# Kernel optimization log

Hardware: AMD Instinct MI355X
Metric: run time of the kernel (lower is better)

The kernel has to match this reference:

```python
import jax, jax.numpy as jnp
import numpy as np

B, N, C, H = 8, 1568, 384, 6
D = C // H
SCALE = D ** -0.5
EPS = 1e-6


def setup_inputs() -> dict:
    key = jax.random.key(0)
    k1, k2, k3, k4 = jax.random.split(key, 4)
    x = jax.random.normal(k1, (B, N, C), dtype=jnp.float32)
    # binary token-keep policy (0/1), as produced by the pruning module
    vis_tube = jax.random.randint(k2, (B, N, 1), 0, 2).astype(jnp.float32)
    w_qkv = jax.random.normal(k3, (3 * C, C), dtype=jnp.float32) * (C ** -0.5)
    w_proj = jax.random.normal(k4, (C, C), dtype=jnp.float32) * (C ** -0.5)
    b_proj = jnp.zeros((C,), dtype=jnp.float32)
    return {"x": x, "vis_tube": vis_tube, "w_qkv": w_qkv, "w_proj": w_proj, "b_proj": b_proj}


def _attn_forward(x, vis_tube, w_qkv, w_proj, b_proj):
    qkv = (x @ w_qkv.T).reshape(B, N, 3, H, D)
    qkv = jnp.transpose(qkv, (2, 0, 3, 1, 4))  # [3,B,H,N,D]
    q, k, v = qkv[0], qkv[1], qkv[2]

    attn = jnp.einsum('bhnd,bhmd->bhnm', q, k) * SCALE  # [B,H,N,N]

    # softmax_with_policy: mask keys by policy, but always keep the diagonal
    policy = vis_tube.reshape(B, 1, 1, N)
    eye = jnp.eye(N, dtype=policy.dtype).reshape(1, 1, N, N)
    attn_policy = policy + (1.0 - policy) * eye  # [B,1,N,N]

    max_att = jnp.max(attn, axis=-1, keepdims=True)
    e = jnp.exp(attn - max_att) * attn_policy
    attn = (e + EPS / N) / (jnp.sum(e, axis=-1, keepdims=True) + EPS)

    out = jnp.einsum('bhnm,bhmd->bhnd', attn, v)  # [B,H,N,D]
    out = jnp.transpose(out, (0, 2, 1, 3)).reshape(B, N, C)
    return out @ w_proj.T + b_proj


def reference(x, vis_tube, w_qkv, w_proj, b_proj):
    return _attn_forward(x, vis_tube, w_qkv, w_proj, b_proj)
```

## Files before the change

kernel.cpp:

```cpp
#include <hip/hip_runtime.h>

#define B_ 8
#define N_ 1568
#define NPAD_ 1600
#define C_ 384
#define H_ 6
#define D_ 64
#define BH_ 48
#define SZ_ (B_*H_*N_*D_)
#define EPS_ 1e-6f
#define CSC_ 0.18033688011112042f

typedef short s16x8 __attribute__((ext_vector_type(8)));
typedef short s16x4 __attribute__((ext_vector_type(4)));
typedef float f32x4 __attribute__((ext_vector_type(4)));

static __device__ __forceinline__ ushort f2bf(float f){
  union { float f; unsigned u; } v; v.f = f;
  unsigned r = v.u + 0x7fffu + ((v.u >> 16) & 1u);
  return (ushort)(r >> 16);
}
static __device__ __forceinline__ unsigned cvtpk(float lo, float hi){
  unsigned r;
  asm("v_cvt_pk_bf16_f32 %0, %1, %2" : "=v"(r) : "v"(lo), "v"(hi));
  return r;
}
#define MFMA16(a,b,c) __builtin_amdgcn_mfma_f32_16x16x32_bf16((a),(b),(c),0,0,0)

#if __has_builtin(__builtin_amdgcn_exp2f)
#define EXP2F(x) __builtin_amdgcn_exp2f(x)
#else
#define EXP2F(x) exp2f(x)
#endif

#define POLPAD_ (B_*NPAD_)
__global__ __launch_bounds__(256) void pol_pad_k(const float* __restrict__ vis, float* __restrict__ pp){
  int i = blockIdx.x*256 + threadIdx.x;
  if (i < POLPAD_){
    int b = i / NPAD_, n = i - b*NPAD_;
    pp[i] = (n < N_) ? vis[b*N_ + n] : 0.f;
  }
}

#define XV8_ 602112
#define WQ8_ 55296
#define WP8_ 18432
__global__ __launch_bounds__(256) void cvt_all(const float* __restrict__ X, const float* __restrict__ Wq,
                                               const float* __restrict__ Wp, ushort* __restrict__ Xb,
                                               ushort* __restrict__ Wqb, ushort* __restrict__ Wpb){
  int i = blockIdx.x*256 + threadIdx.x;
  const float* src; ushort* dst; int off;
  if (i < XV8_)            { src = X;  dst = Xb;  off = i; }
  else if (i < XV8_+WQ8_)  { src = Wq; dst = Wqb; off = i - XV8_; }
  else                     { src = Wp; dst = Wpb; off = i - XV8_ - WQ8_; }
  float4 a = ((const float4*)src)[off*2];
  float4 b = ((const float4*)src)[off*2+1];
  s16x8 r;
  r[0]=(short)f2bf(a.x); r[1]=(short)f2bf(a.y); r[2]=(short)f2bf(a.z); r[3]=(short)f2bf(a.w);
  r[4]=(short)f2bf(b.x); r[5]=(short)f2bf(b.y); r[6]=(short)f2bf(b.z); r[7]=(short)f2bf(b.w);
  *(s16x8*)&dst[off*8] = r;
}

__global__ __launch_bounds__(256) void qkv_gemm(const ushort* __restrict__ Xb, const ushort* __restrict__ Wb,
                                                ushort* __restrict__ Qg, ushort* __restrict__ Kg,
                                                ushort* __restrict__ Vtg){
  __shared__ __align__(16) ushort Al[128*40];
  __shared__ __align__(16) ushort Bl[128*40];
  const int tid = threadIdx.x, lane = tid&63, w = tid>>6;
  const int g = lane>>4, lr = lane&15;
  const int wr = w>>1, wc = w&1;
  const int m0 = blockIdx.x*128, j0 = blockIdx.y*128;
  const int ar = tid>>1, ah = tid&1;
  f32x4 acc[4][4];
  #pragma unroll
  for (int i=0;i<4;i++)
    #pragma unroll
    for (int j=0;j<4;j++) acc[i][j]=(f32x4){0,0,0,0};

  for (int ks=0; ks<384; ks+=32){
    const ushort* as = Xb + (size_t)(m0+ar)*384 + ks + ah*16;
    s16x8 a0 = ((const s16x8*)as)[0];
    s16x8 a1 = ((const s16x8*)as)[1];
    const ushort* bs = Wb + (size_t)(j0+ar)*384 + ks + ah*16;
    s16x8 b0 = ((const s16x8*)bs)[0];
    s16x8 b1 = ((const s16x8*)bs)[1];
    *(s16x8*)&Al[ar*40 + ah*16]     = a0;
    *(s16x8*)&Al[ar*40 + ah*16 + 8] = a1;
    *(s16x8*)&Bl[ar*40 + ah*16]     = b0;
    *(s16x8*)&Bl[ar*40 + ah*16 + 8] = b1;
    __syncthreads();
    s16x8 af[4], bf[4];
    #pragma unroll
    for (int fm=0; fm<4; fm++) af[fm] = *(const s16x8*)&Al[(wr*64+fm*16+lr)*40 + g*8];
    #pragma unroll
    for (int fn=0; fn<4; fn++) bf[fn] = *(const s16x8*)&Bl[(wc*64+fn*16+lr)*40 + g*8];
    #pragma unroll
    for (int fm=0; fm<4; fm++)
      #pragma unroll
      for (int fn=0; fn<4; fn++)
        acc[fm][fn] = MFMA16(af[fm], bf[fn], acc[fm][fn]);
    __syncthreads();
  }
  #pragma unroll
  for (int fm=0; fm<4; fm++){
    #pragma unroll
    for (int jj=0; jj<4; jj++){
      int m = m0 + wr*64 + fm*16 + g*4 + jj;
      int bi = m / N_; int n = m - bi*N_;
      #pragma unroll
      for (int fn=0; fn<4; fn++){
        int j = j0 + wc*64 + fn*16 + lr;
        int t = j/384, jc = j - t*384;
        int h = jc>>6, d = jc&63;
        float v = acc[fm][fn][jj];
        if (t==0)      Qg[((size_t)(bi*H_+h)*N_ + n)*64 + d] = f2bf(v * CSC_);
        else if (t==1) Kg[((size_t)(bi*H_+h)*N_ + n)*64 + d] = f2bf(v);
        else           Vtg[((size_t)(bi*H_+h)*64 + d)*N_ + n] = f2bf(v);
      }
    }
  }
}

#define LOADK(D0,D1,TT) do{ \
  _Pragma("unroll") \
  for (int kg=0;kg<4;kg++){ \
    int kr = (TT)+kg*16+lr; kr = kr<N_?kr:N_-1; \
    const ushort* kp = Kbh + (size_t)kr*64; \
    D0[kg] = *(const s16x8*)(kp + g*8); \
    D1[kg] = *(const s16x8*)(kp + 32 + g*8); } }while(0)

#define LOADV(TT) do{ \
  _Pragma("unroll") \
  for (int fd=0;fd<4;fd++){ \
    const ushort* vp = Vbh + (size_t)(fd*16+lr)*N_ + (TT); \
    va0_[fd] = *(const s16x8*)(vp + g*8); \
    va1_[fd] = *(const s16x8*)(vp + 32 + g*8); } }while(0)

#define LOADP(TT) do{ \
  _Pragma("unroll") \
  for (int kg=0;kg<4;kg++) pmv[kg] = *(const float4*)&polp[(TT) + kg*16 + 4*g]; }while(0)

#define PROC(KC0,KC1,QF0,QF1,OO,MM,LL,QQ,DG,T0) do{ \
  f32x4 st[4]; \
  _Pragma("unroll") \
  for (int kg=0;kg<4;kg++){ f32x4 z=(f32x4){0,0,0,0}; z=MFMA16(KC0[kg],QF0,z); st[kg]=MFMA16(KC1[kg],QF1,z); } \
  float pmax; { \
    float x0=fmaxf(fmaxf(st[0][0],st[0][1]),fmaxf(st[0][2],st[0][3])); \
    float x1=fmaxf(fmaxf(st[1][0],st[1][1]),fmaxf(st[1][2],st[1][3])); \
    float x2=fmaxf(fmaxf(st[2][0],st[2][1]),fmaxf(st[2][2],st[2][3])); \
    float x3=fmaxf(fmaxf(st[3][0],st[3][1]),fmaxf(st[3][2],st[3][3])); \
    pmax=fmaxf(fmaxf(x0,x1),fmaxf(x2,x3)); \
    pmax=fmaxf(pmax,__shfl_xor(pmax,16)); pmax=fmaxf(pmax,__shfl_xor(pmax,32)); } \
  if (__any(pmax > (MM)+8.f)){ \
    float Mn=fmaxf((MM),pmax); float corr=EXP2F((MM)-Mn); (LL)*=corr; \
    _Pragma("unroll") for (int fd=0;fd<4;fd++){ OO[fd][0]*=corr;OO[fd][1]*=corr;OO[fd][2]*=corr;OO[fd][3]*=corr; } \
    (MM)=Mn; } \
  _Pragma("unroll") \
  for (int kg=0;kg<4;kg++){ \
    _Pragma("unroll") \
    for (int jj=0;jj<4;jj++){ \
      float e=EXP2F(st[kg][jj]-(MM)); float em=e*((&pmv[kg].x)[jj]); \
      int key=(T0)+kg*16+4*g+jj; \
      st[kg][jj]=((DG)&&key==(QQ))?e:em; } } \
  { float se=(st[0][0]+st[0][1])+(st[0][2]+st[0][3]); \
    se+=(st[1][0]+st[1][1])+(st[1][2]+st[1][3]); \
    se+=(st[2][0]+st[2][1])+(st[2][2]+st[2][3]); \
    se+=(st[3][0]+st[3][1])+(st[3][2]+st[3][3]); \
    se+=__shfl_xor(se,16); se+=__shfl_xor(se,32); (LL)+=se; } \
  unsigned pk[4][2]; \
  _Pragma("unroll") \
  for (int kg=0;kg<4;kg++){ pk[kg][0]=cvtpk(st[kg][0],st[kg][1]); pk[kg][1]=cvtpk(st[kg][2],st[kg][3]); } \
  union { unsigned u[4]; s16x8 v; } bfr[2]; \
  _Pragma("unroll") \
  for (int kh=0;kh<2;kh++){ \
    _Pragma("unroll") \
    for (int wd=0;wd<4;wd++){ \
      int srcl=(wd<2)?sl0:sl1; \
      unsigned q0_=(unsigned)__shfl((int)pk[2*kh][wd&1],srcl); \
      unsigned q1_=(unsigned)__shfl((int)pk[2*kh+1][wd&1],srcl); \
      bfr[kh].u[wd]=(g<2)?q0_:q1_; } } \
  _Pragma("unroll") \
  for (int fd=0;fd<4;fd++){ OO[fd]=MFMA16(va0_[fd],bfr[0].v,OO[fd]); OO[fd]=MFMA16(va1_[fd],bfr[1].v,OO[fd]); } \
}while(0)

__global__ __launch_bounds__(256,2) void attn_fwd(const ushort* __restrict__ Qg, const ushort* __restrict__ Kg,
                                                  const ushort* __restrict__ Vt, const float* __restrict__ pol,
                                                  ushort* __restrict__ AO){
  const int tid = threadIdx.x, lane = tid&63, w = tid>>6;
  const int g = lane>>4, lr = lane&15;
  const int bh = blockIdx.x; const int b = bh / H_, h = bh - b*H_;
  const int qbase = blockIdx.y*128 + w*32;
  const int qA = qbase + lr, qB = qbase + 16 + lr;
  const int qAc = qA < N_ ? qA : N_-1;
  const int qBc = qB < N_ ? qB : N_-1;
  const ushort* QrA = Qg + ((size_t)bh*N_ + qAc)*64;
  const ushort* QrB = Qg + ((size_t)bh*N_ + qBc)*64;
  const s16x8 qa0 = *(const s16x8*)(QrA + g*8);
  const s16x8 qa1 = *(const s16x8*)(QrA + 32 + g*8);
  const s16x8 qb0 = *(const s16x8*)(QrB + g*8);
  const s16x8 qb1 = *(const s16x8*)(QrB + 32 + g*8);
  const float* polp = pol + b*NPAD_;
  const ushort* Kbh = Kg + (size_t)bh*N_*64;
  const ushort* Vbh = Vt + (size_t)bh*64*N_;
  const int sl0 = ((lane>>4)&1)<<5 | lr;
  const int sl1 = sl0 + 16;
  const int dbase = qbase & ~63;

  f32x4 oA[4], oB[4];
  #pragma unroll
  for (int i=0;i<4;i++){ oA[i]=(f32x4){0,0,0,0}; oB[i]=(f32x4){0,0,0,0}; }
  float MA=-INFINITY, LA=0.f, MB=-INFINITY, LB=0.f;

  s16x8 ka0[4], ka1[4], kb0[4], kb1[4], va0_[4], va1_[4];
  float4 pmv[4];

  LOADK(ka0, ka1, 0);
  #pragma unroll 1
  for (int it=0; it<12; it++){
    const int t0 = it*128;
    LOADV(t0); LOADP(t0);
    LOADK(kb0, kb1, t0+64);
    PROC(ka0,ka1, qa0,qa1, oA,MA,LA,qA, (dbase==t0), t0);
    PROC(ka0,ka1, qb0,qb1, oB,MB,LB,qB, (dbase==t0), t0);
    const int t1 = t0+64;
    LOADV(t1); LOADP(t1);
    LOADK(ka0, ka1, t1+64);
    PROC(kb0,kb1, qa0,qa1, oA,MA,LA,qA, (dbase==t1), t1);
    PROC(kb0,kb1, qb0,qb1, oB,MB,LB,qB, (dbase==t1), t1);
  }
  {
    const int t0 = 1536;
    LOADV(t0); LOADP(t0);
    PROC(ka0,ka1, qa0,qa1, oA,MA,LA,qA, (dbase==t0), t0);
    PROC(ka0,ka1, qb0,qb1, oB,MB,LB,qB, (dbase==t0), t0);
  }

  if (qA < N_){
    float inv = 1.f / (LA + EPS_);
    ushort* aop = AO + ((size_t)b*N_ + qA)*C_ + h*64 + 4*g;
    #pragma unroll
    for (int fd=0; fd<4; fd++){
      s16x4 r;
      r[0]=(short)f2bf(oA[fd][0]*inv); r[1]=(short)f2bf(oA[fd][1]*inv);
      r[2]=(short)f2bf(oA[fd][2]*inv); r[3]=(short)f2bf(oA[fd][3]*inv);
      *(s16x4*)(aop + fd*16) = r;
    }
  }
  if (qB < N_){
    float inv = 1.f / (LB + EPS_);
    ushort* aop = AO + ((size_t)b*N_ + qB)*C_ + h*64 + 4*g;
    #pragma unroll
    for (int fd=0; fd<4; fd++){
      s16x4 r;
      r[0]=(short)f2bf(oB[fd][0]*inv); r[1]=(short)f2bf(oB[fd][1]*inv);
      r[2]=(short)f2bf(oB[fd][2]*inv); r[3]=(short)f2bf(oB[fd][3]*inv);
      *(s16x4*)(aop + fd*16) = r;
    }
  }
}

__global__ __launch_bounds__(256) void proj_gemm(const ushort* __restrict__ A, const ushort* __restrict__ Wb,
                                                 const float* __restrict__ bias, float* __restrict__ out){
  __shared__ __align__(16) ushort Al[128*40];
  __shared__ __align__(16) ushort Bl[128*40];
  const int tid = threadIdx.x, lane = tid&63, w = tid>>6;
  const int g = lane>>4, lr = lane&15;
  const int wr = w>>1, wc = w&1;
  const int m0 = blockIdx.x*128, j0 = blockIdx.y*128;
  const int ar = tid>>1, ah = tid&1;
  f32x4 acc[4][4];
  #pragma unroll
  for (int i=0;i<4;i++)
    #pragma unroll
    for (int j=0;j<4;j++) acc[i][j]=(f32x4){0,0,0,0};

  for (int ks=0; ks<384; ks+=32){
    const ushort* as = A + (size_t)(m0+ar)*384 + ks + ah*16;
    s16x8 a0 = ((const s16x8*)as)[0];
    s16x8 a1 = ((const s16x8*)as)[1];
    const ushort* bs = Wb + (size_t)(j0+ar)*384 + ks + ah*16;
    s16x8 b0 = ((const s16x8*)bs)[0];
    s16x8 b1 = ((const s16x8*)bs)[1];
    *(s16x8*)&Al[ar*40 + ah*16]     = a0;
    *(s16x8*)&Al[ar*40 + ah*16 + 8] = a1;
    *(s16x8*)&Bl[ar*40 + ah*16]     = b0;
    *(s16x8*)&Bl[ar*40 + ah*16 + 8] = b1;
    __syncthreads();
    s16x8 af[4], bf[4];
    #pragma unroll
    for (int fm=0; fm<4; fm++) af[fm] = *(const s16x8*)&Al[(wr*64+fm*16+lr)*40 + g*8];
    #pragma unroll
    for (int fn=0; fn<4; fn++) bf[fn] = *(const s16x8*)&Bl[(wc*64+fn*16+lr)*40 + g*8];
    #pragma unroll
    for (int fm=0; fm<4; fm++)
      #pragma unroll
      for (int fn=0; fn<4; fn++)
        acc[fm][fn] = MFMA16(af[fm], bf[fn], acc[fm][fn]);
    __syncthreads();
  }
  float bsv[4];
  #pragma unroll
  for (int fn=0; fn<4; fn++) bsv[fn] = bias[j0 + wc*64 + fn*16 + lr];
  #pragma unroll
  for (int fm=0; fm<4; fm++){
    #pragma unroll
    for (int jj=0; jj<4; jj++){
      int m = m0 + wr*64 + fm*16 + g*4 + jj;
      #pragma unroll
      for (int fn=0; fn<4; fn++){
        int j = j0 + wc*64 + fn*16 + lr;
        out[(size_t)m*384 + j] = acc[fm][fn][jj] + bsv[fn];
      }
    }
  }
}

extern "C" void kernel_launch(void* const* d_in, const int* in_sizes, int n_in,
                              void* d_out, int out_size, void* d_ws, size_t ws_size,
                              hipStream_t stream) {
  const float* x     = (const float*)d_in[0];
  const float* vis   = (const float*)d_in[1];
  const float* wqkv  = (const float*)d_in[2];
  const float* wproj = (const float*)d_in[3];
  const float* bproj = (const float*)d_in[4];
  float* out = (float*)d_out;

  ushort* Qg  = (ushort*)d_ws;
  ushort* Kg  = Qg + SZ_;
  ushort* Vtg = Kg + SZ_;
  ushort* AO  = Vtg + SZ_;
  ushort* Xb  = AO;
  ushort* Wqb = AO + SZ_;
  ushort* Wpb = Wqb + 3*C_*C_;
  float*  pol_pad = (float*)(Wpb + C_*C_);

  pol_pad_k<<<(POLPAD_+255)/256, 256, 0, stream>>>(vis, pol_pad);
  cvt_all<<<2640, 256, 0, stream>>>(x, wqkv, wproj, Xb, Wqb, Wpb);
  qkv_gemm<<<dim3(98,9), 256, 0, stream>>>(Xb, Wqb, Qg, Kg, Vtg);
  attn_fwd<<<dim3(48,13), 256, 0, stream>>>(Qg, Kg, Vtg, pol_pad, AO);
  proj_gemm<<<dim3(98,3), 256, 0, stream>>>(AO, Wpb, bproj, out);
}
```

Before: 253.6 us.

## Use single-wave attention blocks, add V transpose kernel, set MFMA priorities

The attention kernel goes from 256-thread blocks covering 128 queries to 64-thread blocks covering 32 queries, giving a 48x49 grid. Since 1568 = 49*32, the query bounds checks and clamps can be dropped. When the workspace is large enough, the QKV GEMM now writes V row-major and a separate small kernel transposes it through LDS, replacing the strided scattered Vt stores. The attention inner loop also gains s_setprio raises around the MFMA sections and sched_barrier fences after the loads. These changes add one extra kernel launch and a round-trip of V through memory.

```diff
diff --git a/kernel.cpp b/kernel.cpp
--- a/kernel.cpp
+++ b/kernel.cpp
@@ -63,7 +63,8 @@
 
 __global__ __launch_bounds__(256) void qkv_gemm(const ushort* __restrict__ Xb, const ushort* __restrict__ Wb,
                                                 ushort* __restrict__ Qg, ushort* __restrict__ Kg,
-                                                ushort* __restrict__ Vtg){
+                                                ushort* __restrict__ Vg, ushort* __restrict__ Vtg,
+                                                int vmode){
   __shared__ __align__(16) ushort Al[128*40];
   __shared__ __align__(16) ushort Bl[128*40];
   const int tid = threadIdx.x, lane = tid&63, w = tid>>6;
@@ -115,10 +116,27 @@
         float v = acc[fm][fn][jj];
         if (t==0)      Qg[((size_t)(bi*H_+h)*N_ + n)*64 + d] = f2bf(v * CSC_);
         else if (t==1) Kg[((size_t)(bi*H_+h)*N_ + n)*64 + d] = f2bf(v);
-        else           Vtg[((size_t)(bi*H_+h)*64 + d)*N_ + n] = f2bf(v);
+        else {
+          if (vmode) Vg[((size_t)(bi*H_+h)*N_ + n)*64 + d] = f2bf(v);
+          else       Vtg[((size_t)(bi*H_+h)*64 + d)*N_ + n] = f2bf(v);
+        }
       }
     }
   }
+}
+
+__global__ __launch_bounds__(256) void v_tr(const ushort* __restrict__ Vg, ushort* __restrict__ Vt){
+  __shared__ ushort lds[32*72];
+  const int bh = blockIdx.x, k0 = blockIdx.y*32;
+  const int tid = threadIdx.x;
+  const int r = tid>>3, dc = (tid&7)*8;
+  *(s16x8*)&lds[r*72 + dc] = *(const s16x8*)&Vg[((size_t)bh*N_ + k0 + r)*64 + dc];
+  __syncthreads();
+  const int d = tid>>2, kc = (tid&3)*8;
+  s16x8 o;
+  #pragma unroll
+  for (int i=0;i<8;i++) o[i] = (short)lds[(kc+i)*72 + d];
+  *(s16x8*)&Vt[((size_t)bh*64 + d)*N_ + k0 + kc] = o;
 }
 
 #define LOADK(D0,D1,TT) do{ \
@@ -142,8 +160,10 @@
 
 #define PROC(KC0,KC1,QF0,QF1,OO,MM,LL,QQ,DG,T0) do{ \
   f32x4 st[4]; \
+  __builtin_amdgcn_s_setprio(1); \
   _Pragma("unroll") \
   for (int kg=0;kg<4;kg++){ f32x4 z=(f32x4){0,0,0,0}; z=MFMA16(KC0[kg],QF0,z); st[kg]=MFMA16(KC1[kg],QF1,z); } \
+  __builtin_amdgcn_s_setprio(0); \
   float pmax; { \
     float x0=fmaxf(fmaxf(st[0][0],st[0][1]),fmaxf(st[0][2],st[0][3])); \
     float x1=fmaxf(fmaxf(st[1][0],st[1][1]),fmaxf(st[1][2],st[1][3])); \
@@ -179,22 +199,22 @@
       unsigned q0_=(unsigned)__shfl((int)pk[2*kh][wd&1],srcl); \
       unsigned q1_=(unsigned)__shfl((int)pk[2*kh+1][wd&1],srcl); \
       bfr[kh].u[wd]=(g<2)?q0_:q1_; } } \
+  __builtin_amdgcn_s_setprio(1); \
   _Pragma("unroll") \
   for (int fd=0;fd<4;fd++){ OO[fd]=MFMA16(va0_[fd],bfr[0].v,OO[fd]); OO[fd]=MFMA16(va1_[fd],bfr[1].v,OO[fd]); } \
+  __builtin_amdgcn_s_setprio(0); \
 }while(0)
 
-__global__ __launch_bounds__(256,2) void attn_fwd(const ushort* __restrict__ Qg, const ushort* __restrict__ Kg,
-                                                  const ushort* __restrict__ Vt, const float* __restrict__ pol,
-                                                  ushort* __restrict__ AO){
-  const int tid = threadIdx.x, lane = tid&63, w = tid>>6;
+__global__ __launch_bounds__(64,2) void attn_fwd(const ushort* __restrict__ Qg, const ushort* __restrict__ Kg,
+                                                 const ushort* __restrict__ Vt, const float* __restrict__ pol,
+                                                 ushort* __restrict__ AO){
+  const int lane = threadIdx.x & 63;
   const int g = lane>>4, lr = lane&15;
   const int bh = blockIdx.x; const int b = bh / H_, h = bh - b*H_;
-  const int qbase = blockIdx.y*128 + w*32;
+  const int qbase = blockIdx.y*32;
   const int qA = qbase + lr, qB = qbase + 16 + lr;
-  const int qAc = qA < N_ ? qA : N_-1;
-  const int qBc = qB < N_ ? qB : N_-1;
-  const ushort* QrA = Qg + ((size_t)bh*N_ + qAc)*64;
-  const ushort* QrB = Qg + ((size_t)bh*N_ + qBc)*64;
+  const ushort* QrA = Qg + ((size_t)bh*N_ + qA)*64;
+  const ushort* QrB = Qg + ((size_t)bh*N_ + qB)*64;
   const s16x8 qa0 = *(const s16x8*)(QrA + g*8);
   const s16x8 qa1 = *(const s16x8*)(QrA + 32 + g*8);
   const s16x8 qb0 = *(const s16x8*)(QrB + g*8);
@@ -220,11 +240,13 @@
     const int t0 = it*128;
     LOADV(t0); LOADP(t0);
     LOADK(kb0, kb1, t0+64);
+    __builtin_amdgcn_sched_barrier(0);
     PROC(ka0,ka1, qa0,qa1, oA,MA,LA,qA, (dbase==t0), t0);
     PROC(ka0,ka1, qb0,qb1, oB,MB,LB,qB, (dbase==t0), t0);
     const int t1 = t0+64;
     LOADV(t1); LOADP(t1);
     LOADK(ka0, ka1, t1+64);
+    __builtin_amdgcn_sched_barrier(0);
     PROC(kb0,kb1, qa0,qa1, oA,MA,LA,qA, (dbase==t1), t1);
     PROC(kb0,kb1, qb0,qb1, oB,MB,LB,qB, (dbase==t1), t1);
   }
@@ -235,7 +257,7 @@
     PROC(ka0,ka1, qb0,qb1, oB,MB,LB,qB, (dbase==t0), t0);
   }
 
-  if (qA < N_){
+  {
     float inv = 1.f / (LA + EPS_);
     ushort* aop = AO + ((size_t)b*N_ + qA)*C_ + h*64 + 4*g;
     #pragma unroll
@@ -246,7 +268,7 @@
       *(s16x4*)(aop + fd*16) = r;
     }
   }
-  if (qB < N_){
+  {
     float inv = 1.f / (LB + EPS_);
     ushort* aop = AO + ((size_t)b*N_ + qB)*C_ + h*64 + 4*g;
     #pragma unroll
@@ -330,13 +352,17 @@
   ushort* Vtg = Kg + SZ_;
   ushort* AO  = Vtg + SZ_;
   ushort* Xb  = AO;
-  ushort* Wqb = AO + SZ_;
+  ushort* Vg  = AO + SZ_;
+  size_t need_tr = (size_t)5*SZ_*2 + (size_t)(3*C_*C_ + C_*C_)*2 + (size_t)POLPAD_*4;
+  int tr = (ws_size >= need_tr) ? 1 : 0;
+  ushort* Wqb = tr ? (Vg + SZ_) : (Vg);
   ushort* Wpb = Wqb + 3*C_*C_;
   float*  pol_pad = (float*)(Wpb + C_*C_);
 
   pol_pad_k<<<(POLPAD_+255)/256, 256, 0, stream>>>(vis, pol_pad);
   cvt_all<<<2640, 256, 0, stream>>>(x, wqkv, wproj, Xb, Wqb, Wpb);
-  qkv_gemm<<<dim3(98,9), 256, 0, stream>>>(Xb, Wqb, Qg, Kg, Vtg);
-  attn_fwd<<<dim3(48,13), 256, 0, stream>>>(Qg, Kg, Vtg, pol_pad, AO);
+  qkv_gemm<<<dim3(98,9), 256, 0, stream>>>(Xb, Wqb, Qg, Kg, Vg, Vtg, tr);
+  if (tr) v_tr<<<dim3(48,49), 256, 0, stream>>>(Vg, Vtg);
+  attn_fwd<<<dim3(48,49), 64, 0, stream>>>(Qg, Kg, Vtg, pol_pad, AO);
   proj_gemm<<<dim3(98,3), 256, 0, stream>>>(AO, Wpb, bproj, out);
 }
```

Measured after the change: 252.2 us. About the same (-0.5%).
